# Optimization experiments

Hardware: AMD Instinct MI355X
Metric: run time of the kernel (lower is better)

## Reference

```python
import jax, jax.numpy as jnp
import numpy as np

B, N, D, L = 32, 512, 768, 4  # batch, nodes (incl. CLS at last index), in_dim==hidden_size, num_layers


def setup_inputs() -> dict:
    key = jax.random.key(0)
    ks = jax.random.split(key, 6)
    feature = jax.random.normal(ks[0], (B, N, D), jnp.float32)
    # token mask: random valid lengths, CLS node at the last index always present
    lengths = jax.random.randint(ks[1], (B,), N // 2, N)
    pmask = (jnp.arange(N)[None, :] < lengths[:, None]).astype(jnp.float32)
    pmask = pmask.at[:, -1].set(1.0)
    # L2C (learning-to-connect) bilinear gate params, one pair per layer
    Wq = jax.random.normal(ks[2], (L, D, D), jnp.float32) / np.sqrt(D)
    Wk = jax.random.normal(ks[3], (L, D, D), jnp.float32) / np.sqrt(D)
    # attention-pool projection Linear(in_dim, 1)
    proj_w = jax.random.normal(ks[4], (D,), jnp.float32) / np.sqrt(D)
    proj_b = jnp.zeros((), jnp.float32)
    return dict(pmask=pmask, feature=feature, Wq=Wq, Wk=Wk, proj_w=proj_w, proj_b=proj_b)


def reference(pmask, feature, Wq, Wk, proj_w, proj_b):
    full_adj = pmask[:, :, None] * pmask[:, None, :]        # [B,N,N]
    full_sum = jnp.sum(full_adj) + 1e-8
    p_sum = pmask.sum(-1)                                    # [B]
    scale = 1.0 / np.sqrt(D)
    preds = [feature]
    adjs, c_list, g_list = [], [], []
    total_l0 = jnp.zeros((), feature.dtype)
    for l in range(L):
        # L2C: bilinear sigmoid gate masked by full adjacency, L0-style loss = mean gate mass
        q = jnp.einsum('bnd,de->bne', feature, Wq[l])
        k = jnp.einsum('bnd,de->bne', feature, Wk[l])
        adj = jax.nn.sigmoid(jnp.einsum('bne,bme->bnm', q, k) * scale) * full_adj  # [B,N,N]
        total_l0 = total_l0 + jnp.sum(adj) / full_sum
        # sparse_statistics: CLS-row sparsity and graph-edge sparsity
        c_list.append(adj[:, -1, :-1].sum(-1) / p_sum)               # [B]
        g_list.append(adj[:, :-1, :-1].sum((-1, -2)) / p_sum ** 2)   # [B]
        adjs.append(adj)
        # symmetric degree normalization: D^-1/2 A D^-1/2 (diag bmm == row/col scaling)
        deg = adj.sum(2)                                              # [B,N]
        dis = jnp.where(deg > 0, jax.lax.rsqrt(jnp.maximum(deg, 1e-12)), 0.0)
        dis = jax.lax.stop_gradient(dis)                              # .detach() in original
        adj_n = dis[:, :, None] * adj * dis[:, None, :]
        # feature = adj_^T @ feature
        feature = jnp.einsum('bnm,bnd->bmd', adj_n, feature)
        preds.append(feature)
    pps = jnp.stack(preds, axis=2)                                    # [B,N,L+1,D]
    retain = jax.nn.sigmoid(jnp.einsum('bnld,d->bnl', pps, proj_w) + proj_b)  # [B,N,L+1]
    out = jnp.einsum('bnl,bnld->bnd', retain, pps)                    # [B,N,D]
    c_sparsity = jnp.stack(c_list, axis=-1)                           # [B,L]
    g_sparsity = jnp.stack(g_list, axis=-1)                           # [B,L]
    return (out, retain, jnp.stack(adjs, axis=-1), total_l0 / L, c_sparsity, g_sparsity)
```

## Files before the change

### kernel.cpp

```cpp
#include <hip/hip_runtime.h>

typedef short s16x8 __attribute__((ext_vector_type(8)));
typedef float f32x4 __attribute__((ext_vector_type(4)));

constexpr int BATCH = 32, NODES = 512, DIM = 768, LAYERS = 4;
constexpr float QK_SCALE = 0.03608439182435161f;

constexpr size_t OUT_OFF  = 0;
constexpr size_t RET_OFF  = (size_t)BATCH * NODES * DIM;
constexpr size_t ADJS_OFF = RET_OFF + (size_t)BATCH * NODES * (LAYERS + 1);
constexpr size_t L0_OFF   = ADJS_OFF + (size_t)BATCH * NODES * NODES * LAYERS;
constexpr size_t C_OFF    = L0_OFF + 1;
constexpr size_t G_OFF    = C_OFF + BATCH * LAYERS;

#define DEVI static __device__ __forceinline__

DEVI float bf2f(unsigned short u) {
    union { unsigned int i; float f; } v; v.i = ((unsigned int)u) << 16; return v.f;
}
DEVI unsigned short f2bf(float f) {
    union { float f; unsigned int i; } v; v.f = f;
    return (unsigned short)((v.i + 0x7FFFu + ((v.i >> 16) & 1u)) >> 16);
}
DEVI ushort4 pk4(float4 v) {
    ushort4 o; o.x = f2bf(v.x); o.y = f2bf(v.y); o.z = f2bf(v.z); o.w = f2bf(v.w); return o;
}
DEVI float sigm(float x) { return 1.0f / (1.0f + __expf(-x)); }
DEVI float deg2dis(float d) { return d > 0.f ? rsqrtf(fmaxf(d, 1e-12f)) : 0.f; }

DEVI void gload16(const unsigned short* g, unsigned short* l) {
    __builtin_amdgcn_global_load_lds(
        (const __attribute__((address_space(1))) unsigned int*)g,
        (__attribute__((address_space(3))) unsigned int*)l, 16, 0, 0);
}

__global__ __launch_bounds__(256) void gemm_nt_small(
    const unsigned short* __restrict__ A0, const unsigned short* __restrict__ B0,
    unsigned short* __restrict__ C0,
    int K, int lda, int ldb, int ldc,
    long sA, long sB, long sC)
{
    __shared__ __align__(16) unsigned short As[128 * 32];
    __shared__ __align__(16) unsigned short Bs[128 * 32];

    const int tid  = threadIdx.x;
    const int lane = tid & 63;
    const int wave = tid >> 6;
    const int wr = (wave >> 1) << 6;
    const int wc = (wave & 1) << 6;
    const int z = blockIdx.z;
    const int rows0 = blockIdx.x << 7;
    const int cols0 = blockIdx.y << 7;

    const unsigned short* A = A0 + (size_t)z * sA + (size_t)rows0 * lda;
    const unsigned short* Bsrc = B0 + (size_t)z * sB + (size_t)cols0 * ldb;

    f32x4 acc[4][4] = {};

    const int srow = wave * 16 + (lane >> 2);
    const int scb  = (lane & 3) << 3;
    const unsigned short* Ag = A + (size_t)srow * lda + scb;
    const unsigned short* Bg = Bsrc + (size_t)srow * ldb + scb;
    unsigned short* lA0 = &As[wave * 512];
    unsigned short* lA1 = &As[2048 + wave * 512];
    unsigned short* lB0 = &Bs[wave * 512];
    unsigned short* lB1 = &Bs[2048 + wave * 512];
    const size_t a64 = (size_t)64 * lda, b64 = (size_t)64 * ldb;

    const int mrow = lane & 15;
    const int kq   = (lane >> 4) << 3;

    for (int kt = 0; kt < K; kt += 32) {
        __syncthreads();
        gload16(Ag + kt, lA0);
        gload16(Ag + a64 + kt, lA1);
        gload16(Bg + kt, lB0);
        gload16(Bg + b64 + kt, lB1);
        __syncthreads();

        s16x8 af[4], bfr[4];
        #pragma unroll
        for (int i = 0; i < 4; ++i) {
            af[i]  = *(const s16x8*)(&As[(wr + i * 16 + mrow) * 32 + kq]);
            bfr[i] = *(const s16x8*)(&Bs[(wc + i * 16 + mrow) * 32 + kq]);
        }
        #pragma unroll
        for (int i = 0; i < 4; ++i)
            #pragma unroll
            for (int j = 0; j < 4; ++j)
                acc[i][j] = __builtin_amdgcn_mfma_f32_16x16x32_bf16(af[i], bfr[j], acc[i][j], 0, 0, 0);
    }

    const int colb = lane & 15, quad = lane >> 4;
    unsigned short* C = C0 + (size_t)z * sC;
    #pragma unroll
    for (int i = 0; i < 4; ++i) {
        const int rbase = rows0 + wr + i * 16 + (quad << 2);
        #pragma unroll
        for (int j = 0; j < 4; ++j) {
            const int cc = cols0 + wc + j * 16 + colb;
            #pragma unroll
            for (int r = 0; r < 4; ++r)
                C[(size_t)(rbase + r) * ldc + cc] = f2bf(acc[i][j][r]);
        }
    }
}

template <int MODE>
__global__ __launch_bounds__(512) void gemm256_nt(
    const unsigned short* __restrict__ A0, const unsigned short* __restrict__ B0,
    unsigned short* __restrict__ C0,
    int K, int lda, int ldb, int ldc,
    long sA, long sB, long sC,
    const float* __restrict__ pmask, float* __restrict__ deg,
    unsigned short* __restrict__ adjT,
    float* __restrict__ l0_acc, float* __restrict__ c_acc, float* __restrict__ g_acc,
    int layer)
{
    __shared__ __align__(16) unsigned short lds[2][2][2][8192];
    __shared__ float pmr[256];
    __shared__ float pmc[256];

    const int tid  = threadIdx.x;
    const int lane = tid & 63;
    const int wave = tid >> 6;
    const int wm   = wave >> 2;
    const int wn   = wave & 3;
    const int z = blockIdx.z;
    const int rows0 = blockIdx.x << 8;
    const int cols0 = blockIdx.y << 8;

    const unsigned short* A = A0 + (size_t)z * sA;
    const unsigned short* B = B0 + (size_t)z * sB;

    if constexpr (MODE == 1) {
        if (tid < 256) pmr[tid] = pmask[(size_t)z * NODES + rows0 + tid];
        else pmc[tid - 256] = pmask[(size_t)z * NODES + cols0 + (tid - 256)];
    }

    const int srow  = lane >> 3;
    const int scol8 = (lane & 7) ^ srow;

    auto stage_half = [&](int T, int op, int h) {
        const int base = (op == 0) ? rows0 : cols0;
        const int ld   = (op == 0) ? lda : ldb;
        const unsigned short* src = ((op == 0) ? A : B)
            + (size_t)(base + h * 128 + wave * 8 + srow) * ld + (size_t)T * 64 + scol8 * 8;
        unsigned short* dst = &lds[T & 1][op][h][wave * 512];
        gload16(src, dst);
        gload16(src + (size_t)64 * ld, dst + 4096);
    };

    const int nkt = K >> 6;

    stage_half(0, 0, 0); stage_half(0, 0, 1);
    stage_half(0, 1, 0); stage_half(0, 1, 1);
    if (nkt > 1) {
        stage_half(1, 0, 0);
        asm volatile("s_waitcnt vmcnt(2)" ::: "memory");
    } else {
        asm volatile("s_waitcnt vmcnt(0)" ::: "memory");
    }
    __builtin_amdgcn_s_barrier();
    asm volatile("" ::: "memory");

    f32x4 acc[8][4] = {};

    const int fr = lane & 15;
    const int fq = lane >> 4;
    const int xk = (fr & 7) << 4;
    const int frow64 = fr * 64;
    const int ka0 = ((fq * 16) ^ xk) >> 1;
    const int ka1 = ((64 + fq * 16) ^ xk) >> 1;
    const int brow = (wn & 1) * 4096;

    for (int T = 0; T < nkt; ++T) {
        const unsigned short* Ah = &lds[T & 1][0][wm][0];
        const unsigned short* Bh = &lds[T & 1][1][wn >> 1][0];
        s16x8 af[4][2], bq[4][2];

        #pragma unroll
        for (int i = 0; i < 4; ++i) {
            af[i][0] = *(const s16x8*)(Ah + i * 1024 + frow64 + ka0);
            af[i][1] = *(const s16x8*)(Ah + i * 1024 + frow64 + ka1);
        }
        #pragma unroll
        for (int j = 0; j < 2; ++j) {
            bq[j][0] = *(const s16x8*)(Bh + brow + j * 1024 + frow64 + ka0);
            bq[j][1] = *(const s16x8*)(Bh + brow + j * 1024 + frow64 + ka1);
        }
        if (T + 1 < nkt) stage_half(T + 1, 0, 1);
        asm volatile("" ::: "memory");
        __builtin_amdgcn_s_barrier();
        asm volatile("s_waitcnt lgkmcnt(0)" ::: "memory");
        __builtin_amdgcn_sched_barrier(0);
        __builtin_amdgcn_s_setprio(1);
        #pragma unroll
        for (int i = 0; i < 4; ++i)
            #pragma unroll
            for (int j = 0; j < 2; ++j)
                #pragma unroll
                for (int s = 0; s < 2; ++s)
                    acc[i][j] = __builtin_amdgcn_mfma_f32_16x16x32_bf16(af[i][s], bq[j][s], acc[i][j], 0, 0, 0);
        __builtin_amdgcn_s_setprio(0);
        asm volatile("" ::: "memory");
        __builtin_amdgcn_s_barrier();
        asm volatile("" ::: "memory");

        #pragma unroll
        for (int j = 0; j < 2; ++j) {
            bq[2 + j][0] = *(const s16x8*)(Bh + brow + (2 + j) * 1024 + frow64 + ka0);
            bq[2 + j][1] = *(const s16x8*)(Bh + brow + (2 + j) * 1024 + frow64 + ka1);
        }
        if (T + 1 < nkt) stage_half(T + 1, 1, 0);
        asm volatile("" ::: "memory");
        __builtin_amdgcn_s_barrier();
        asm volatile("s_waitcnt lgkmcnt(0)" ::: "memory");
        __builtin_amdgcn_sched_barrier(0);
        __builtin_amdgcn_s_setprio(1);
        #pragma unroll
        for (int i = 0; i < 4; ++i)
            #pragma unroll
            for (int j = 2; j < 4; ++j)
                #pragma unroll
                for (int s = 0; s < 2; ++s)
                    acc[i][j] = __builtin_amdgcn_mfma_f32_16x16x32_bf16(af[i][s], bq[j][s], acc[i][j], 0, 0, 0);
        __builtin_amdgcn_s_setprio(0);
        asm volatile("" ::: "memory");
        __builtin_amdgcn_s_barrier();
        asm volatile("" ::: "memory");

        #pragma unroll
        for (int i = 0; i < 4; ++i) {
            af[i][0] = *(const s16x8*)(Ah + (4 + i) * 1024 + frow64 + ka0);
            af[i][1] = *(const s16x8*)(Ah + (4 + i) * 1024 + frow64 + ka1);
        }
        if (T + 1 < nkt) stage_half(T + 1, 1, 1);
        asm volatile("" ::: "memory");
        __builtin_amdgcn_s_barrier();
        asm volatile("s_waitcnt lgkmcnt(0)" ::: "memory");
        __builtin_amdgcn_sched_barrier(0);
        __builtin_amdgcn_s_setprio(1);
        #pragma unroll
        for (int i = 0; i < 4; ++i)
            #pragma unroll
            for (int j = 2; j < 4; ++j)
                #pragma unroll
                for (int s = 0; s < 2; ++s)
                    acc[4 + i][j] = __builtin_amdgcn_mfma_f32_16x16x32_bf16(af[i][s], bq[j][s], acc[4 + i][j], 0, 0, 0);
        __builtin_amdgcn_s_setprio(0);
        asm volatile("" ::: "memory");
        __builtin_amdgcn_s_barrier();
        asm volatile("" ::: "memory");

        if (T + 2 < nkt) stage_half(T + 2, 0, 0);
        asm volatile("" ::: "memory");
        __builtin_amdgcn_s_barrier();
        asm volatile("" ::: "memory");
        __builtin_amdgcn_s_setprio(1);
        #pragma unroll
        for (int i = 0; i < 4; ++i)
            #pragma unroll
            for (int j = 0; j < 2; ++j)
                #pragma unroll
                for (int s = 0; s < 2; ++s)
                    acc[4 + i][j] = __builtin_amdgcn_mfma_f32_16x16x32_bf16(af[i][s], bq[j][s], acc[4 + i][j], 0, 0, 0);
        __builtin_amdgcn_s_setprio(0);
        if (T + 2 < nkt) asm volatile("s_waitcnt vmcnt(2)" ::: "memory");
        else             asm volatile("s_waitcnt vmcnt(0)" ::: "memory");
        __builtin_amdgcn_s_barrier();
        asm volatile("" ::: "memory");
    }

    const int quad4 = fq << 2;

    if constexpr (MODE != 1) {
        unsigned short* C = C0 + (size_t)z * sC;
        #pragma unroll
        for (int i = 0; i < 8; ++i) {
            const int rbase = rows0 + wm * 128 + i * 16 + quad4;
            float dv[4];
            if constexpr (MODE == 2) {
                #pragma unroll
                for (int r = 0; r < 4; ++r) dv[r] = deg2dis(deg[(size_t)z * NODES + rbase + r]);
            }
            #pragma unroll
            for (int j = 0; j < 4; ++j) {
                const int cc = cols0 + wn * 64 + j * 16 + fr;
                #pragma unroll
                for (int r = 0; r < 4; ++r) {
                    float v = acc[i][j][r];
                    if constexpr (MODE == 2) v *= dv[r];
                    C[(size_t)(rbase + r) * ldc + cc] = f2bf(v);
                }
            }
        }
    } else {
        float tot = 0.f, gs = 0.f, cs = 0.f;
        #pragma unroll
        for (int i = 0; i < 8; ++i) {
            const int nloc = wm * 128 + i * 16 + quad4;
            #pragma unroll
            for (int r = 0; r < 4; ++r) {
                const int n = rows0 + nloc + r;
                const float pmn = pmr[nloc + r];
                float dp = 0.f;
                #pragma unroll
                for (int j = 0; j < 4; ++j) {
                    const int mloc = wn * 64 + j * 16 + fr;
                    const int m = cols0 + mloc;
                    float a = pmn * pmc[mloc] * sigm(acc[i][j][r] * QK_SCALE);
                    acc[i][j][r] = a;
                    dp += a;
                    tot += a;
                    if (m < NODES - 1) {
                        if (n < NODES - 1) gs += a;
                        else cs += a;
                    }
                }
                dp += __shfl_xor(dp, 1, 16);
                dp += __shfl_xor(dp, 2, 16);
                dp += __shfl_xor(dp, 4, 16);
                dp += __shfl_xor(dp, 8, 16);
                if (fr == 0) atomicAdd(&deg[(size_t)z * NODES + n], dp);
            }
        }
        #pragma unroll
        for (int i = 0; i < 8; ++i) {
            const int nb = rows0 + wm * 128 + i * 16 + quad4;
            #pragma unroll
            for (int j = 0; j < 4; ++j) {
                const int m = cols0 + wn * 64 + j * 16 + fr;
                ushort4 pk;
                pk.x = f2bf(acc[i][j][0]); pk.y = f2bf(acc[i][j][1]);
                pk.z = f2bf(acc[i][j][2]); pk.w = f2bf(acc[i][j][3]);
                *(ushort4*)(adjT + ((size_t)z * NODES + m) * NODES + nb) = pk;
            }
        }
        #pragma unroll
        for (int o = 1; o < 64; o <<= 1) {
            tot += __shfl_xor(tot, o, 64);
            gs  += __shfl_xor(gs, o, 64);
            cs  += __shfl_xor(cs, o, 64);
        }
        if (lane == 0) {
            atomicAdd(l0_acc, tot);
            atomicAdd(&g_acc[z * LAYERS + layer], gs);
            atomicAdd(&c_acc[z * LAYERS + layer], cs);
        }
    }
}

__global__ __launch_bounds__(256) void interleave_adjs(
    const unsigned short* __restrict__ adjT, float* __restrict__ adjs)
{
    __shared__ unsigned short t[4][32][36];
    const int b = blockIdx.z, m0 = blockIdx.x << 5, n0 = blockIdx.y << 5;
    const int tr = threadIdx.x >> 3, tc = (threadIdx.x & 7) << 2;
    #pragma unroll
    for (int l = 0; l < LAYERS; ++l) {
        ushort4 v = *(const ushort4*)(adjT + (((size_t)l * BATCH + b) * NODES + m0 + tr) * NODES + n0 + tc);
        t[l][tr][tc] = v.x; t[l][tr][tc + 1] = v.y; t[l][tr][tc + 2] = v.z; t[l][tr][tc + 3] = v.w;
    }
    __syncthreads();
    float* dst = adjs + (((size_t)b * NODES + n0 + tr) * NODES + m0 + tc) * LAYERS;
    #pragma unroll
    for (int mm = 0; mm < 4; ++mm) {
        float4 f;
        f.x = bf2f(t[0][tc + mm][tr]); f.y = bf2f(t[1][tc + mm][tr]);
        f.z = bf2f(t[2][tc + mm][tr]); f.w = bf2f(t[3][tc + mm][tr]);
        *(float4*)(dst + mm * 4) = f;
    }
}

__global__ void fp_transpose(const unsigned short* __restrict__ X, const float* __restrict__ deg,
                             unsigned short* __restrict__ fpt)
{
    __shared__ unsigned short t[32][36];
    const int b = blockIdx.z;
    const int n0 = blockIdx.x << 5, d0 = blockIdx.y << 5;
    const int tr = threadIdx.x >> 3, tc = (threadIdx.x & 7) << 2;
    const float dv = deg2dis(deg[(size_t)b * NODES + n0 + tr]);
    ushort4 v = *(const ushort4*)(X + ((size_t)b * NODES + n0 + tr) * DIM + d0 + tc);
    t[tr][tc]     = f2bf(bf2f(v.x) * dv);
    t[tr][tc + 1] = f2bf(bf2f(v.y) * dv);
    t[tr][tc + 2] = f2bf(bf2f(v.z) * dv);
    t[tr][tc + 3] = f2bf(bf2f(v.w) * dv);
    __syncthreads();
    ushort4 o;
    o.x = t[tc + 0][tr]; o.y = t[tc + 1][tr]; o.z = t[tc + 2][tr]; o.w = t[tc + 3][tr];
    *(ushort4*)(fpt + ((size_t)b * DIM + d0 + tr) * NODES + n0 + tc) = o;
}

__global__ void cast_all(const float* __restrict__ feat, const float* __restrict__ Wq,
                         const float* __restrict__ Wk, unsigned short* __restrict__ featb,
                         unsigned short* __restrict__ Wqb, unsigned short* __restrict__ Wkb,
                         const float* __restrict__ pm, float* __restrict__ ps)
{
    const int bx = blockIdx.x;
    if (bx >= 16896) {
        const int b = bx - 16896, t = threadIdx.x;
        float s = pm[(size_t)b * NODES + t] + pm[(size_t)b * NODES + 256 + t];
        #pragma unroll
        for (int o = 1; o < 64; o <<= 1) s += __shfl_xor(s, o, 64);
        __shared__ float sh[4];
        if ((t & 63) == 0) sh[t >> 6] = s;
        __syncthreads();
        if (t == 0) ps[b] = sh[0] + sh[1] + sh[2] + sh[3];
        return;
    }
    const float* src; unsigned short* dst; size_t base;
    if (bx < 12288)      { src = feat; dst = featb; base = (size_t)bx * 1024; }
    else if (bx < 14592) { src = Wq;   dst = Wqb;   base = (size_t)(bx - 12288) * 1024; }
    else                 { src = Wk;   dst = Wkb;   base = (size_t)(bx - 14592) * 1024; }
    const size_t i = base + ((size_t)threadIdx.x << 2);
    float4 v = *(const float4*)(src + i);
    *(ushort4*)(dst + i) = pk4(v);
}

__global__ __launch_bounds__(256) void final_out(
    const float* __restrict__ X0f, const unsigned short* __restrict__ X1,
    const unsigned short* __restrict__ X2, const unsigned short* __restrict__ X3,
    const unsigned short* __restrict__ X4,
    const float* __restrict__ pw, const float* __restrict__ pb,
    const float* __restrict__ ps, const float* __restrict__ c_acc,
    const float* __restrict__ g_acc, const float* __restrict__ l0,
    float* __restrict__ ob)
{
    if (blockIdx.x == 0) {
        const int t = threadIdx.x;
        if (t < BATCH * LAYERS) {
            const int b = t >> 2;
            const float p = ps[b];
            ob[C_OFF + t] = c_acc[t] / p;
            ob[G_OFF + t] = g_acc[t] / (p * p);
        }
        if (t == 0) {
            float fs = 1e-8f;
            for (int b = 0; b < BATCH; ++b) fs += ps[b] * ps[b];
            ob[L0_OFF] = l0[0] / (fs * (float)LAYERS);
        }
    }

    const int row = (blockIdx.x << 2) + (threadIdx.x >> 6);
    const int lane = threadIdx.x & 63;
    const unsigned short* Xb[4] = { X1 + (size_t)row * DIM, X2 + (size_t)row * DIM,
                                    X3 + (size_t)row * DIM, X4 + (size_t)row * DIM };
    float xs[5][12];
    float dot[5] = {};
    #pragma unroll
    for (int c = 0; c < 3; ++c) {
        const int idx = c * 256 + (lane << 2);
        float4 wv = *(const float4*)(pw + idx);
        float4 x0 = *(const float4*)(X0f + (size_t)row * DIM + idx);
        xs[0][c * 4 + 0] = x0.x; xs[0][c * 4 + 1] = x0.y;
        xs[0][c * 4 + 2] = x0.z; xs[0][c * 4 + 3] = x0.w;
        dot[0] += x0.x * wv.x + x0.y * wv.y + x0.z * wv.z + x0.w * wv.w;
        #pragma unroll
        for (int l = 0; l < 4; ++l) {
            ushort4 xv = *(const ushort4*)(Xb[l] + idx);
            float a0 = bf2f(xv.x), a1 = bf2f(xv.y), a2 = bf2f(xv.z), a3 = bf2f(xv.w);
            xs[l + 1][c * 4 + 0] = a0; xs[l + 1][c * 4 + 1] = a1;
            xs[l + 1][c * 4 + 2] = a2; xs[l + 1][c * 4 + 3] = a3;
            dot[l + 1] += a0 * wv.x + a1 * wv.y + a2 * wv.z + a3 * wv.w;
        }
    }
    #pragma unroll
    for (int l = 0; l < 5; ++l)
        #pragma unroll
        for (int o = 1; o < 64; o <<= 1) dot[l] += __shfl_xor(dot[l], o, 64);
    const float pbv = pb[0];
    float r[5];
    #pragma unroll
    for (int l = 0; l < 5; ++l) r[l] = sigm(dot[l] + pbv);
    if (lane == 0) {
        float* rr = ob + RET_OFF + (size_t)row * (LAYERS + 1);
        rr[0] = r[0]; rr[1] = r[1]; rr[2] = r[2]; rr[3] = r[3]; rr[4] = r[4];
    }
    float* orow = ob + OUT_OFF + (size_t)row * DIM;
    #pragma unroll
    for (int c = 0; c < 3; ++c) {
        float4 p;
        p.x = r[0] * xs[0][c * 4 + 0]; p.y = r[0] * xs[0][c * 4 + 1];
        p.z = r[0] * xs[0][c * 4 + 2]; p.w = r[0] * xs[0][c * 4 + 3];
        #pragma unroll
        for (int l = 1; l < 5; ++l) {
            p.x += r[l] * xs[l][c * 4 + 0]; p.y += r[l] * xs[l][c * 4 + 1];
            p.z += r[l] * xs[l][c * 4 + 2]; p.w += r[l] * xs[l][c * 4 + 3];
        }
        *(float4*)(orow + c * 256 + (lane << 2)) = p;
    }
}

extern "C" void kernel_launch(void* const* d_in, const int* in_sizes, int n_in,
                              void* d_out, int out_size, void* d_ws, size_t ws_size,
                              hipStream_t stream)
{
    (void)in_sizes; (void)n_in; (void)out_size; (void)ws_size;
    const float* pmask = (const float*)d_in[0];
    const float* feat  = (const float*)d_in[1];
    const float* Wq    = (const float*)d_in[2];
    const float* Wk    = (const float*)d_in[3];
    const float* projw = (const float*)d_in[4];
    const float* projb = (const float*)d_in[5];
    float* ob = (float*)d_out;

    char* w = (char*)d_ws;
    unsigned short* Xb[4];
    Xb[0] = (unsigned short*)(w + 0);
    Xb[1] = (unsigned short*)(w + 25165824);
    Xb[2] = (unsigned short*)(w + 50331648);
    Xb[3] = (unsigned short*)(w + 75497472);
    unsigned short* qws   = (unsigned short*)(w + 100663296);
    unsigned short* featb = (unsigned short*)(w + 125829120);
    unsigned short* adjT  = (unsigned short*)(w + 150994944);
    unsigned short* Wqb   = (unsigned short*)(w + 218103808);
    unsigned short* Wkb   = (unsigned short*)(w + 222822400);
    unsigned short* MT    = (unsigned short*)(w + 227540992);
    float* deg_all = (float*)(w + 232259584);
    float* c_acc   = (float*)(w + 232521728);
    float* g_acc   = (float*)(w + 232522240);
    float* l0_acc  = (float*)(w + 232522752);
    float* p_sum   = (float*)(w + 232523008);

    dim3 blk(256);
    dim3 blk5(512);
    hipMemsetAsync(w + 232259584, 0, 263680, stream);

    cast_all<<<dim3(16928), blk, 0, stream>>>(feat, Wq, Wk, featb, Wqb, Wkb, pmask, p_sum);

    gemm_nt_small<<<dim3(6, 6, 4), blk, 0, stream>>>(
        Wkb, Wqb, MT, DIM, DIM, DIM, DIM,
        (long)DIM * DIM, (long)DIM * DIM, (long)DIM * DIM);

    for (int l = 0; l < LAYERS; ++l) {
        float* deg_l = deg_all + (size_t)l * BATCH * NODES;
        unsigned short* adjT_l = adjT + (size_t)l * BATCH * NODES * NODES;
        const unsigned short* Xsrc = (l == 0) ? featb : Xb[l - 1];

        gemm_nt_small<<<dim3(128, 6, 1), blk, 0, stream>>>(
            Xsrc, MT + (size_t)l * DIM * DIM, qws,
            DIM, DIM, DIM, DIM, 0L, 0L, 0L);

        gemm256_nt<1><<<dim3(2, 2, 32), blk5, 0, stream>>>(
            qws, Xsrc, nullptr,
            DIM, DIM, DIM, 0, (long)NODES * DIM, (long)NODES * DIM, 0L,
            pmask, deg_l, adjT_l, l0_acc, c_acc, g_acc, l);

        fp_transpose<<<dim3(16, 24, 32), blk, 0, stream>>>(Xsrc, deg_l, qws);

        gemm256_nt<2><<<dim3(2, 3, 32), blk5, 0, stream>>>(
            adjT_l, qws, Xb[l],
            NODES, NODES, NODES, DIM, (long)NODES * NODES, (long)DIM * NODES, (long)NODES * DIM,
            nullptr, deg_l, nullptr, nullptr, nullptr, nullptr, 0);
    }

    interleave_adjs<<<dim3(16, 16, 32), blk, 0, stream>>>(adjT, ob + ADJS_OFF);
    final_out<<<dim3(4096), blk, 0, stream>>>(feat, Xb[0], Xb[1], Xb[2], Xb[3],
                                              projw, projb, p_sum, c_acc, g_acc, l0_acc, ob);
}
```

Before: 789.3 us.

## Fuse per-layer GEMM and transpose stages into one cooperative persistent kernel

```diff
diff --git a/kernel.cpp b/kernel.cpp
--- a/kernel.cpp
+++ b/kernel.cpp
@@ -1,4 +1,7 @@
 #include <hip/hip_runtime.h>
+#include <hip/hip_cooperative_groups.h>
+
+namespace cg = cooperative_groups;
 
 typedef short s16x8 __attribute__((ext_vector_type(8)));
 typedef float f32x4 __attribute__((ext_vector_type(4)));
@@ -107,35 +110,24 @@
 }
 
 template <int MODE>
-__global__ __launch_bounds__(512) void gemm256_nt(
-    const unsigned short* __restrict__ A0, const unsigned short* __restrict__ B0,
-    unsigned short* __restrict__ C0,
-    int K, int lda, int ldb, int ldc,
-    long sA, long sB, long sC,
-    const float* __restrict__ pmask, float* __restrict__ deg,
-    unsigned short* __restrict__ adjT,
-    float* __restrict__ l0_acc, float* __restrict__ c_acc, float* __restrict__ g_acc,
-    int layer)
+__device__ __forceinline__ void gemm_tile(
+    unsigned short* __restrict__ ldsb, float* __restrict__ pmr, float* __restrict__ pmc,
+    const unsigned short* __restrict__ A, const unsigned short* __restrict__ B,
+    unsigned short* __restrict__ C,
+    int K, int lda, int ldb, int ldc, int rows0, int cols0,
+    const float* __restrict__ pmz, float* __restrict__ degz,
+    unsigned short* __restrict__ adjz,
+    float* __restrict__ l0p, float* __restrict__ cp, float* __restrict__ gp)
 {
-    __shared__ __align__(16) unsigned short lds[2][2][2][8192];
-    __shared__ float pmr[256];
-    __shared__ float pmc[256];
-
     const int tid  = threadIdx.x;
     const int lane = tid & 63;
     const int wave = tid >> 6;
     const int wm   = wave >> 2;
     const int wn   = wave & 3;
-    const int z = blockIdx.z;
-    const int rows0 = blockIdx.x << 8;
-    const int cols0 = blockIdx.y << 8;
-
-    const unsigned short* A = A0 + (size_t)z * sA;
-    const unsigned short* B = B0 + (size_t)z * sB;
 
     if constexpr (MODE == 1) {
-        if (tid < 256) pmr[tid] = pmask[(size_t)z * NODES + rows0 + tid];
-        else pmc[tid - 256] = pmask[(size_t)z * NODES + cols0 + (tid - 256)];
+        if (tid < 256) pmr[tid] = pmz[rows0 + tid];
+        else pmc[tid - 256] = pmz[cols0 + (tid - 256)];
     }
 
     const int srow  = lane >> 3;
@@ -146,7 +138,7 @@
         const int ld   = (op == 0) ? lda : ldb;
         const unsigned short* src = ((op == 0) ? A : B)
             + (size_t)(base + h * 128 + wave * 8 + srow) * ld + (size_t)T * 64 + scol8 * 8;
-        unsigned short* dst = &lds[T & 1][op][h][wave * 512];
+        unsigned short* dst = ldsb + (size_t)(((T & 1) << 2) + (op << 1) + h) * 8192 + wave * 512;
         gload16(src, dst);
         gload16(src + (size_t)64 * ld, dst + 4096);
     };
@@ -175,8 +167,8 @@
     const int brow = (wn & 1) * 4096;
 
     for (int T = 0; T < nkt; ++T) {
-        const unsigned short* Ah = &lds[T & 1][0][wm][0];
-        const unsigned short* Bh = &lds[T & 1][1][wn >> 1][0];
+        const unsigned short* Ah = ldsb + (size_t)(((T & 1) << 2) + wm) * 8192;
+        const unsigned short* Bh = ldsb + (size_t)(((T & 1) << 2) + 2 + (wn >> 1)) * 8192;
         s16x8 af[4][2], bq[4][2];
 
         #pragma unroll
@@ -275,14 +267,13 @@
     const int quad4 = fq << 2;
 
     if constexpr (MODE != 1) {
-        unsigned short* C = C0 + (size_t)z * sC;
         #pragma unroll
         for (int i = 0; i < 8; ++i) {
             const int rbase = rows0 + wm * 128 + i * 16 + quad4;
             float dv[4];
             if constexpr (MODE == 2) {
                 #pragma unroll
-                for (int r = 0; r < 4; ++r) dv[r] = deg2dis(deg[(size_t)z * NODES + rbase + r]);
+                for (int r = 0; r < 4; ++r) dv[r] = deg2dis(degz[rbase + r]);
             }
             #pragma unroll
             for (int j = 0; j < 4; ++j) {
@@ -322,7 +313,7 @@
                 dp += __shfl_xor(dp, 2, 16);
                 dp += __shfl_xor(dp, 4, 16);
                 dp += __shfl_xor(dp, 8, 16);
-                if (fr == 0) atomicAdd(&deg[(size_t)z * NODES + n], dp);
+                if (fr == 0) atomicAdd(&degz[n], dp);
             }
         }
         #pragma unroll
@@ -334,7 +325,7 @@
                 ushort4 pk;
                 pk.x = f2bf(acc[i][j][0]); pk.y = f2bf(acc[i][j][1]);
                 pk.z = f2bf(acc[i][j][2]); pk.w = f2bf(acc[i][j][3]);
-                *(ushort4*)(adjT + ((size_t)z * NODES + m) * NODES + nb) = pk;
+                *(ushort4*)(adjz + (size_t)m * NODES + nb) = pk;
             }
         }
         #pragma unroll
@@ -344,10 +335,103 @@
             cs  += __shfl_xor(cs, o, 64);
         }
         if (lane == 0) {
-            atomicAdd(l0_acc, tot);
-            atomicAdd(&g_acc[z * LAYERS + layer], gs);
-            atomicAdd(&c_acc[z * LAYERS + layer], cs);
-        }
+            atomicAdd(l0p, tot);
+            atomicAdd(gp, gs);
+            atomicAdd(cp, cs);
+        }
+    }
+}
+
+__global__ __launch_bounds__(512) void layers_coop(
+    const unsigned short* __restrict__ featb,
+    unsigned short* __restrict__ qws,
+    const unsigned short* __restrict__ MT,
+    unsigned short* __restrict__ adjT,
+    unsigned short* __restrict__ X0, unsigned short* __restrict__ X1,
+    unsigned short* __restrict__ X2, unsigned short* __restrict__ X3,
+    const float* __restrict__ pmask, float* __restrict__ deg_all,
+    float* __restrict__ l0_acc, float* __restrict__ c_acc, float* __restrict__ g_acc)
+{
+    __shared__ __align__(16) unsigned short lds[2][2][2][8192];
+    __shared__ float pmr[256];
+    __shared__ float pmc[256];
+
+    cg::grid_group grid = cg::this_grid();
+    const int bid = blockIdx.x;
+    const int tid = threadIdx.x;
+    unsigned short* ldsb = &lds[0][0][0][0];
+    unsigned short* const Xout[4] = { X0, X1, X2, X3 };
+
+    for (int l = 0; l < LAYERS; ++l) {
+        const unsigned short* Xsrc = (l == 0) ? featb : Xout[l - 1];
+        float* degl = deg_all + (size_t)l * BATCH * NODES;
+        unsigned short* adjl = adjT + (size_t)l * BATCH * NODES * NODES;
+        const unsigned short* MTl = MT + (size_t)l * DIM * DIM;
+
+        {
+            const int rows0 = (bid / 3) << 8, cols0 = (bid % 3) << 8;
+            gemm_tile<0>(ldsb, pmr, pmc, Xsrc, MTl, qws,
+                         DIM, DIM, DIM, DIM, rows0, cols0,
+                         nullptr, nullptr, nullptr, nullptr, nullptr, nullptr);
+        }
+        grid.sync();
+
+        if (bid < 128) {
+            const int z = bid >> 2;
+            const int rows0 = ((bid >> 1) & 1) << 8, cols0 = (bid & 1) << 8;
+            gemm_tile<1>(ldsb, pmr, pmc,
+                         qws + (size_t)z * NODES * DIM, Xsrc + (size_t)z * NODES * DIM,
+                         nullptr, DIM, DIM, DIM, 0, rows0, cols0,
+                         pmask + (size_t)z * NODES, degl + (size_t)z * NODES,
+                         adjl + (size_t)z * NODES * NODES,
+                         l0_acc, c_acc + z * LAYERS + l, g_acc + z * LAYERS + l);
+        }
+        grid.sync();
+
+        {
+            unsigned short (*ft)[64][72] = (unsigned short (*)[64][72])ldsb;
+            const int tr  = tid >> 3;
+            const int tc8 = (tid & 7) << 3;
+            for (int it = 0; it < 16; it += 2) {
+                #pragma unroll
+                for (int u = 0; u < 2; ++u) {
+                    const int j = bid + (it + u) * 192;
+                    const int z = j / 96, rr = j % 96;
+                    const int n0 = (rr / 12) << 6, d0 = (rr % 12) << 6;
+                    s16x8 v = *(const s16x8*)(Xsrc + ((size_t)z * NODES + n0 + tr) * DIM + d0 + tc8);
+                    const float dv = deg2dis(degl[(size_t)z * NODES + n0 + tr]);
+                    unsigned short* row = &ft[u][tr][tc8];
+                    #pragma unroll
+                    for (int k = 0; k < 8; ++k)
+                        row[k] = f2bf(bf2f((unsigned short)v[k]) * dv);
+                }
+                __syncthreads();
+                #pragma unroll
+                for (int u = 0; u < 2; ++u) {
+                    const int j = bid + (it + u) * 192;
+                    const int z = j / 96, rr = j % 96;
+                    const int n0 = (rr / 12) << 6, d0 = (rr % 12) << 6;
+                    s16x8 o;
+                    #pragma unroll
+                    for (int k = 0; k < 8; ++k) o[k] = (short)ft[u][tc8 + k][tr];
+                    *(s16x8*)(qws + ((size_t)z * DIM + d0 + tr) * NODES + n0 + tc8) = o;
+                }
+                __syncthreads();
+            }
+        }
+        grid.sync();
+
+        {
+            const int z = bid / 6, r = bid % 6;
+            const int rows0 = (r / 3) << 8, cols0 = (r % 3) << 8;
+            gemm_tile<2>(ldsb, pmr, pmc,
+                         adjl + (size_t)z * NODES * NODES, qws + (size_t)z * DIM * NODES,
+                         Xout[l] + (size_t)z * NODES * DIM,
+                         NODES, NODES, NODES, DIM, rows0, cols0,
+                         nullptr, degl + (size_t)z * NODES, nullptr,
+                         nullptr, nullptr, nullptr);
+        }
+        grid.sync();
     }
 }
 
@@ -371,25 +455,6 @@
         f.z = bf2f(t[2][tc + mm][tr]); f.w = bf2f(t[3][tc + mm][tr]);
         *(float4*)(dst + mm * 4) = f;
     }
-}
-
-__global__ void fp_transpose(const unsigned short* __restrict__ X, const float* __restrict__ deg,
-                             unsigned short* __restrict__ fpt)
-{
-    __shared__ unsigned short t[32][36];
-    const int b = blockIdx.z;
-    const int n0 = blockIdx.x << 5, d0 = blockIdx.y << 5;
-    const int tr = threadIdx.x >> 3, tc = (threadIdx.x & 7) << 2;
-    const float dv = deg2dis(deg[(size_t)b * NODES + n0 + tr]);
-    ushort4 v = *(const ushort4*)(X + ((size_t)b * NODES + n0 + tr) * DIM + d0 + tc);
-    t[tr][tc]     = f2bf(bf2f(v.x) * dv);
-    t[tr][tc + 1] = f2bf(bf2f(v.y) * dv);
-    t[tr][tc + 2] = f2bf(bf2f(v.z) * dv);
-    t[tr][tc + 3] = f2bf(bf2f(v.w) * dv);
-    __syncthreads();
-    ushort4 o;
-    o.x = t[tc + 0][tr]; o.y = t[tc + 1][tr]; o.z = t[tc + 2][tr]; o.w = t[tc + 3][tr];
-    *(ushort4*)(fpt + ((size_t)b * DIM + d0 + tr) * NODES + n0 + tc) = o;
 }
 
 __global__ void cast_all(const float* __restrict__ feat, const float* __restrict__ Wq,
@@ -506,11 +571,10 @@
     float* ob = (float*)d_out;
 
     char* w = (char*)d_ws;
-    unsigned short* Xb[4];
-    Xb[0] = (unsigned short*)(w + 0);
-    Xb[1] = (unsigned short*)(w + 25165824);
-    Xb[2] = (unsigned short*)(w + 50331648);
-    Xb[3] = (unsigned short*)(w + 75497472);
+    unsigned short* Xb0 = (unsigned short*)(w + 0);
+    unsigned short* Xb1 = (unsigned short*)(w + 25165824);
+    unsigned short* Xb2 = (unsigned short*)(w + 50331648);
+    unsigned short* Xb3 = (unsigned short*)(w + 75497472);
     unsigned short* qws   = (unsigned short*)(w + 100663296);
     unsigned short* featb = (unsigned short*)(w + 125829120);
     unsigned short* adjT  = (unsigned short*)(w + 150994944);
@@ -524,7 +588,6 @@
     float* p_sum   = (float*)(w + 232523008);
 
     dim3 blk(256);
-    dim3 blk5(512);
     hipMemsetAsync(w + 232259584, 0, 263680, stream);
 
     cast_all<<<dim3(16928), blk, 0, stream>>>(feat, Wq, Wk, featb, Wqb, Wkb, pmask, p_sum);
@@ -533,29 +596,17 @@
         Wkb, Wqb, MT, DIM, DIM, DIM, DIM,
         (long)DIM * DIM, (long)DIM * DIM, (long)DIM * DIM);
 
-    for (int l = 0; l < LAYERS; ++l) {
-        float* deg_l = deg_all + (size_t)l * BATCH * NODES;
-        unsigned short* adjT_l = adjT + (size_t)l * BATCH * NODES * NODES;
-        const unsigned short* Xsrc = (l == 0) ? featb : Xb[l - 1];
-
-        gemm_nt_small<<<dim3(128, 6, 1), blk, 0, stream>>>(
-            Xsrc, MT + (size_t)l * DIM * DIM, qws,
-            DIM, DIM, DIM, DIM, 0L, 0L, 0L);
-
-        gemm256_nt<1><<<dim3(2, 2, 32), blk5, 0, stream>>>(
-            qws, Xsrc, nullptr,
-            DIM, DIM, DIM, 0, (long)NODES * DIM, (long)NODES * DIM, 0L,
-            pmask, deg_l, adjT_l, l0_acc, c_acc, g_acc, l);
-
-        fp_transpose<<<dim3(16, 24, 32), blk, 0, stream>>>(Xsrc, deg_l, qws);
-
-        gemm256_nt<2><<<dim3(2, 3, 32), blk5, 0, stream>>>(
-            adjT_l, qws, Xb[l],
-            NODES, NODES, NODES, DIM, (long)NODES * NODES, (long)DIM * NODES, (long)NODES * DIM,
-            nullptr, deg_l, nullptr, nullptr, nullptr, nullptr, 0);
+    {
+        void* cargs[] = {
+            (void*)&featb, (void*)&qws, (void*)&MT, (void*)&adjT,
+            (void*)&Xb0, (void*)&Xb1, (void*)&Xb2, (void*)&Xb3,
+            (void*)&pmask, (void*)&deg_all,
+            (void*)&l0_acc, (void*)&c_acc, (void*)&g_acc
+        };
+        hipLaunchCooperativeKernel(layers_coop, dim3(192), dim3(512), cargs, 0, stream);
     }
 
     interleave_adjs<<<dim3(16, 16, 32), blk, 0, stream>>>(adjT, ob + ADJS_OFF);
-    final_out<<<dim3(4096), blk, 0, stream>>>(feat, Xb[0], Xb[1], Xb[2], Xb[3],
+    final_out<<<dim3(4096), blk, 0, stream>>>(feat, Xb0, Xb1, Xb2, Xb3,
                                               projw, projb, p_sum, c_acc, g_acc, l0_acc, ob);
 }
```

New measurement: 1.448 ms. 83.5% more time.

## Fuse prologue and tail kernels, compute MT from fp32 weights, use 256-tile GEMM for projection

Applied to the files above, without the earlier changes.

```diff
diff --git a/kernel.cpp b/kernel.cpp
--- a/kernel.cpp
+++ b/kernel.cpp
@@ -32,78 +32,6 @@
     __builtin_amdgcn_global_load_lds(
         (const __attribute__((address_space(1))) unsigned int*)g,
         (__attribute__((address_space(3))) unsigned int*)l, 16, 0, 0);
-}
-
-__global__ __launch_bounds__(256) void gemm_nt_small(
-    const unsigned short* __restrict__ A0, const unsigned short* __restrict__ B0,
-    unsigned short* __restrict__ C0,
-    int K, int lda, int ldb, int ldc,
-    long sA, long sB, long sC)
-{
-    __shared__ __align__(16) unsigned short As[128 * 32];
-    __shared__ __align__(16) unsigned short Bs[128 * 32];
-
-    const int tid  = threadIdx.x;
-    const int lane = tid & 63;
-    const int wave = tid >> 6;
-    const int wr = (wave >> 1) << 6;
-    const int wc = (wave & 1) << 6;
-    const int z = blockIdx.z;
-    const int rows0 = blockIdx.x << 7;
-    const int cols0 = blockIdx.y << 7;
-
-    const unsigned short* A = A0 + (size_t)z * sA + (size_t)rows0 * lda;
-    const unsigned short* Bsrc = B0 + (size_t)z * sB + (size_t)cols0 * ldb;
-
-    f32x4 acc[4][4] = {};
-
-    const int srow = wave * 16 + (lane >> 2);
-    const int scb  = (lane & 3) << 3;
-    const unsigned short* Ag = A + (size_t)srow * lda + scb;
-    const unsigned short* Bg = Bsrc + (size_t)srow * ldb + scb;
-    unsigned short* lA0 = &As[wave * 512];
-    unsigned short* lA1 = &As[2048 + wave * 512];
-    unsigned short* lB0 = &Bs[wave * 512];
-    unsigned short* lB1 = &Bs[2048 + wave * 512];
-    const size_t a64 = (size_t)64 * lda, b64 = (size_t)64 * ldb;
-
-    const int mrow = lane & 15;
-    const int kq   = (lane >> 4) << 3;
-
-    for (int kt = 0; kt < K; kt += 32) {
-        __syncthreads();
-        gload16(Ag + kt, lA0);
-        gload16(Ag + a64 + kt, lA1);
-        gload16(Bg + kt, lB0);
-        gload16(Bg + b64 + kt, lB1);
-        __syncthreads();
-
-        s16x8 af[4], bfr[4];
-        #pragma unroll
-        for (int i = 0; i < 4; ++i) {
-            af[i]  = *(const s16x8*)(&As[(wr + i * 16 + mrow) * 32 + kq]);
-            bfr[i] = *(const s16x8*)(&Bs[(wc + i * 16 + mrow) * 32 + kq]);
-        }
-        #pragma unroll
-        for (int i = 0; i < 4; ++i)
-            #pragma unroll
-            for (int j = 0; j < 4; ++j)
-                acc[i][j] = __builtin_amdgcn_mfma_f32_16x16x32_bf16(af[i], bfr[j], acc[i][j], 0, 0, 0);
-    }
-
-    const int colb = lane & 15, quad = lane >> 4;
-    unsigned short* C = C0 + (size_t)z * sC;
-    #pragma unroll
-    for (int i = 0; i < 4; ++i) {
-        const int rbase = rows0 + wr + i * 16 + (quad << 2);
-        #pragma unroll
-        for (int j = 0; j < 4; ++j) {
-            const int cc = cols0 + wc + j * 16 + colb;
-            #pragma unroll
-            for (int r = 0; r < 4; ++r)
-                C[(size_t)(rbase + r) * ldc + cc] = f2bf(acc[i][j][r]);
-        }
-    }
 }
 
 template <int MODE>
@@ -351,28 +279,6 @@
     }
 }
 
-__global__ __launch_bounds__(256) void interleave_adjs(
-    const unsigned short* __restrict__ adjT, float* __restrict__ adjs)
-{
-    __shared__ unsigned short t[4][32][36];
-    const int b = blockIdx.z, m0 = blockIdx.x << 5, n0 = blockIdx.y << 5;
-    const int tr = threadIdx.x >> 3, tc = (threadIdx.x & 7) << 2;
-    #pragma unroll
-    for (int l = 0; l < LAYERS; ++l) {
-        ushort4 v = *(const ushort4*)(adjT + (((size_t)l * BATCH + b) * NODES + m0 + tr) * NODES + n0 + tc);
-        t[l][tr][tc] = v.x; t[l][tr][tc + 1] = v.y; t[l][tr][tc + 2] = v.z; t[l][tr][tc + 3] = v.w;
-    }
-    __syncthreads();
-    float* dst = adjs + (((size_t)b * NODES + n0 + tr) * NODES + m0 + tc) * LAYERS;
-    #pragma unroll
-    for (int mm = 0; mm < 4; ++mm) {
-        float4 f;
-        f.x = bf2f(t[0][tc + mm][tr]); f.y = bf2f(t[1][tc + mm][tr]);
-        f.z = bf2f(t[2][tc + mm][tr]); f.w = bf2f(t[3][tc + mm][tr]);
-        *(float4*)(dst + mm * 4) = f;
-    }
-}
-
 __global__ void fp_transpose(const unsigned short* __restrict__ X, const float* __restrict__ deg,
                              unsigned short* __restrict__ fpt)
 {
@@ -392,33 +298,116 @@
     *(ushort4*)(fpt + ((size_t)b * DIM + d0 + tr) * NODES + n0 + tc) = o;
 }
 
-__global__ void cast_all(const float* __restrict__ feat, const float* __restrict__ Wq,
-                         const float* __restrict__ Wk, unsigned short* __restrict__ featb,
-                         unsigned short* __restrict__ Wqb, unsigned short* __restrict__ Wkb,
-                         const float* __restrict__ pm, float* __restrict__ ps)
+DEVI void mt_tile(const float* __restrict__ A, const float* __restrict__ B,
+                  unsigned short* __restrict__ C,
+                  unsigned short* As, unsigned short* Bs, int rows0, int cols0)
 {
+    const int tid  = threadIdx.x;
+    const int lane = tid & 63;
+    const int wave = tid >> 6;
+    const int wr = (wave >> 1) << 6;
+    const int wc = (wave & 1) << 6;
+
+    const int srow = wave * 16 + (lane >> 2);
+    const int scb  = (lane & 3) << 3;
+    const float* Ag = A + (size_t)(rows0 + srow) * DIM + scb;
+    const float* Bg = B + (size_t)(cols0 + srow) * DIM + scb;
+    unsigned short* pa = &As[srow * 32 + scb];
+    unsigned short* pb = &Bs[srow * 32 + scb];
+
+    f32x4 acc[4][4] = {};
+    const int mrow = lane & 15;
+    const int kq   = (lane >> 4) << 3;
+
+    for (int kt = 0; kt < DIM; kt += 32) {
+        __syncthreads();
+        float4 a0 = *(const float4*)(Ag + kt);
+        float4 a1 = *(const float4*)(Ag + kt + 4);
+        float4 a2 = *(const float4*)(Ag + (size_t)64 * DIM + kt);
+        float4 a3 = *(const float4*)(Ag + (size_t)64 * DIM + kt + 4);
+        float4 b0 = *(const float4*)(Bg + kt);
+        float4 b1 = *(const float4*)(Bg + kt + 4);
+        float4 b2 = *(const float4*)(Bg + (size_t)64 * DIM + kt);
+        float4 b3 = *(const float4*)(Bg + (size_t)64 * DIM + kt + 4);
+        *(ushort4*)(pa)               = pk4(a0);
+        *(ushort4*)(pa + 4)           = pk4(a1);
+        *(ushort4*)(pa + 64 * 32)     = pk4(a2);
+        *(ushort4*)(pa + 64 * 32 + 4) = pk4(a3);
+        *(ushort4*)(pb)               = pk4(b0);
+        *(ushort4*)(pb + 4)           = pk4(b1);
+        *(ushort4*)(pb + 64 * 32)     = pk4(b2);
+        *(ushort4*)(pb + 64 * 32 + 4) = pk4(b3);
+        __syncthreads();
+
+        s16x8 af[4], bfr[4];
+        #pragma unroll
+        for (int i = 0; i < 4; ++i) {
+            af[i]  = *(const s16x8*)(&As[(wr + i * 16 + mrow) * 32 + kq]);
+            bfr[i] = *(const s16x8*)(&Bs[(wc + i * 16 + mrow) * 32 + kq]);
+        }
+        #pragma unroll
+        for (int i = 0; i < 4; ++i)
+            #pragma unroll
+            for (int j = 0; j < 4; ++j)
+                acc[i][j] = __builtin_amdgcn_mfma_f32_16x16x32_bf16(af[i], bfr[j], acc[i][j], 0, 0, 0);
+    }
+
+    const int colb = lane & 15, quad = lane >> 4;
+    #pragma unroll
+    for (int i = 0; i < 4; ++i) {
+        const int rbase = rows0 + wr + i * 16 + (quad << 2);
+        #pragma unroll
+        for (int j = 0; j < 4; ++j) {
+            const int cc = cols0 + wc + j * 16 + colb;
+            #pragma unroll
+            for (int r = 0; r < 4; ++r)
+                C[(size_t)(rbase + r) * DIM + cc] = f2bf(acc[i][j][r]);
+        }
+    }
+}
+
+__global__ __launch_bounds__(256) void cast_all(
+    const float* __restrict__ feat, const float* __restrict__ Wq,
+    const float* __restrict__ Wk, unsigned short* __restrict__ featb,
+    unsigned short* __restrict__ MT,
+    const float* __restrict__ pm, float* __restrict__ ps,
+    float* __restrict__ zbase)
+{
+    __shared__ __align__(16) unsigned short As[128 * 32];
+    __shared__ __align__(16) unsigned short Bs[128 * 32];
+    __shared__ float sh[4];
+
     const int bx = blockIdx.x;
-    if (bx >= 16896) {
-        const int b = bx - 16896, t = threadIdx.x;
+    if (bx < 12288) {
+        const size_t i = (size_t)bx * 1024 + ((size_t)threadIdx.x << 2);
+        float4 v = *(const float4*)(feat + i);
+        *(ushort4*)(featb + i) = pk4(v);
+        return;
+    }
+    if (bx < 12320) {
+        const int b = bx - 12288, t = threadIdx.x;
         float s = pm[(size_t)b * NODES + t] + pm[(size_t)b * NODES + 256 + t];
         #pragma unroll
         for (int o = 1; o < 64; o <<= 1) s += __shfl_xor(s, o, 64);
-        __shared__ float sh[4];
         if ((t & 63) == 0) sh[t >> 6] = s;
         __syncthreads();
         if (t == 0) ps[b] = sh[0] + sh[1] + sh[2] + sh[3];
         return;
     }
-    const float* src; unsigned short* dst; size_t base;
-    if (bx < 12288)      { src = feat; dst = featb; base = (size_t)bx * 1024; }
-    else if (bx < 14592) { src = Wq;   dst = Wqb;   base = (size_t)(bx - 12288) * 1024; }
-    else                 { src = Wk;   dst = Wkb;   base = (size_t)(bx - 14592) * 1024; }
-    const size_t i = base + ((size_t)threadIdx.x << 2);
-    float4 v = *(const float4*)(src + i);
-    *(ushort4*)(dst + i) = pk4(v);
-}
-
-__global__ __launch_bounds__(256) void final_out(
+    if (bx < 12385) {
+        const int idx = (bx - 12320) * 256 + threadIdx.x;
+        if (idx < 16464) ((float4*)zbase)[idx] = float4{0.f, 0.f, 0.f, 0.f};
+        return;
+    }
+    const int r = bx - 12385;
+    const int z = r / 36, rem = r % 36;
+    mt_tile(Wk + (size_t)z * DIM * DIM, Wq + (size_t)z * DIM * DIM,
+            MT + (size_t)z * DIM * DIM, As, Bs,
+            (rem / 6) << 7, (rem % 6) << 7);
+}
+
+__global__ __launch_bounds__(256) void tail_out(
+    const unsigned short* __restrict__ adjT,
     const float* __restrict__ X0f, const unsigned short* __restrict__ X1,
     const unsigned short* __restrict__ X2, const unsigned short* __restrict__ X3,
     const unsigned short* __restrict__ X4,
@@ -427,7 +416,31 @@
     const float* __restrict__ g_acc, const float* __restrict__ l0,
     float* __restrict__ ob)
 {
-    if (blockIdx.x == 0) {
+    const int bid = blockIdx.x;
+    if (bid < 8192) {
+        __shared__ unsigned short t[4][32][36];
+        float* adjs = ob + ADJS_OFF;
+        const int b = bid >> 8, m0 = (bid & 15) << 5, n0 = ((bid >> 4) & 15) << 5;
+        const int tr = threadIdx.x >> 3, tc = (threadIdx.x & 7) << 2;
+        #pragma unroll
+        for (int l = 0; l < LAYERS; ++l) {
+            ushort4 v = *(const ushort4*)(adjT + (((size_t)l * BATCH + b) * NODES + m0 + tr) * NODES + n0 + tc);
+            t[l][tr][tc] = v.x; t[l][tr][tc + 1] = v.y; t[l][tr][tc + 2] = v.z; t[l][tr][tc + 3] = v.w;
+        }
+        __syncthreads();
+        float* dst = adjs + (((size_t)b * NODES + n0 + tr) * NODES + m0 + tc) * LAYERS;
+        #pragma unroll
+        for (int mm = 0; mm < 4; ++mm) {
+            float4 f;
+            f.x = bf2f(t[0][tc + mm][tr]); f.y = bf2f(t[1][tc + mm][tr]);
+            f.z = bf2f(t[2][tc + mm][tr]); f.w = bf2f(t[3][tc + mm][tr]);
+            *(float4*)(dst + mm * 4) = f;
+        }
+        return;
+    }
+
+    const int fb = bid - 8192;
+    if (fb == 0) {
         const int t = threadIdx.x;
         if (t < BATCH * LAYERS) {
             const int b = t >> 2;
@@ -442,7 +455,7 @@
         }
     }
 
-    const int row = (blockIdx.x << 2) + (threadIdx.x >> 6);
+    const int row = (fb << 2) + (threadIdx.x >> 6);
     const int lane = threadIdx.x & 63;
     const unsigned short* Xb[4] = { X1 + (size_t)row * DIM, X2 + (size_t)row * DIM,
                                     X3 + (size_t)row * DIM, X4 + (size_t)row * DIM };
@@ -514,8 +527,6 @@
     unsigned short* qws   = (unsigned short*)(w + 100663296);
     unsigned short* featb = (unsigned short*)(w + 125829120);
     unsigned short* adjT  = (unsigned short*)(w + 150994944);
-    unsigned short* Wqb   = (unsigned short*)(w + 218103808);
-    unsigned short* Wkb   = (unsigned short*)(w + 222822400);
     unsigned short* MT    = (unsigned short*)(w + 227540992);
     float* deg_all = (float*)(w + 232259584);
     float* c_acc   = (float*)(w + 232521728);
@@ -525,22 +536,19 @@
 
     dim3 blk(256);
     dim3 blk5(512);
-    hipMemsetAsync(w + 232259584, 0, 263680, stream);
-
-    cast_all<<<dim3(16928), blk, 0, stream>>>(feat, Wq, Wk, featb, Wqb, Wkb, pmask, p_sum);
-
-    gemm_nt_small<<<dim3(6, 6, 4), blk, 0, stream>>>(
-        Wkb, Wqb, MT, DIM, DIM, DIM, DIM,
-        (long)DIM * DIM, (long)DIM * DIM, (long)DIM * DIM);
+
+    cast_all<<<dim3(12529), blk, 0, stream>>>(feat, Wq, Wk, featb, MT,
+                                              pmask, p_sum, deg_all);
 
     for (int l = 0; l < LAYERS; ++l) {
         float* deg_l = deg_all + (size_t)l * BATCH * NODES;
         unsigned short* adjT_l = adjT + (size_t)l * BATCH * NODES * NODES;
         const unsigned short* Xsrc = (l == 0) ? featb : Xb[l - 1];
 
-        gemm_nt_small<<<dim3(128, 6, 1), blk, 0, stream>>>(
+        gemm256_nt<0><<<dim3(64, 3, 1), blk5, 0, stream>>>(
             Xsrc, MT + (size_t)l * DIM * DIM, qws,
-            DIM, DIM, DIM, DIM, 0L, 0L, 0L);
+            DIM, DIM, DIM, DIM, 0L, 0L, 0L,
+            nullptr, nullptr, nullptr, nullptr, nullptr, nullptr, 0);
 
         gemm256_nt<1><<<dim3(2, 2, 32), blk5, 0, stream>>>(
             qws, Xsrc, nullptr,
@@ -555,7 +563,6 @@
             nullptr, deg_l, nullptr, nullptr, nullptr, nullptr, 0);
     }
 
-    interleave_adjs<<<dim3(16, 16, 32), blk, 0, stream>>>(adjT, ob + ADJS_OFF);
-    final_out<<<dim3(4096), blk, 0, stream>>>(feat, Xb[0], Xb[1], Xb[2], Xb[3],
+    tail_out<<<dim3(12288), blk, 0, stream>>>(adjT, feat, Xb[0], Xb[1], Xb[2], Xb[3],
                                               projw, projb, p_sum, c_acc, g_acc, l0_acc, ob);
 }
```

Result: no change. 789.3 us (+0.0%).
